# Performance work log

Measured on AMD Instinct MI355X. Metric: run time of the kernel, lower is better.

## Reference

```python
import jax, jax.numpy as jnp
import numpy as np

T, H, I, E, K = 2048, 1024, 768, 16, 4

def setup_inputs() -> dict:
    key = jax.random.key(0)
    k1, k2, k3, k4, k5 = jax.random.split(key, 5)
    hidden_states = jax.random.normal(k1, (T, H), dtype=jnp.float32)
    top_k_index = jax.random.randint(k2, (T, K), 0, E, dtype=jnp.int64)
    top_k_weights = jax.random.uniform(k3, (T, K), dtype=jnp.float32)
    gate_up_proj = jax.random.normal(k4, (E, 2 * I, H), dtype=jnp.float32) * 0.02
    down_proj = jax.random.normal(k5, (E, H, I), dtype=jnp.float32) * 0.02
    return {"hidden_states": hidden_states, "top_k_index": top_k_index,
            "top_k_weights": top_k_weights, "gate_up_proj": gate_up_proj,
            "down_proj": down_proj}

def reference(hidden_states, top_k_index, top_k_weights, gate_up_proj, down_proj):
    # Masked dense MoE: scan over experts, each expert does full-token GEMMs
    # and a per-token combine weight (sum of routing weights where routed to e).
    # index_add over token_idx == sum over k of (mask * weight) * expert_out.
    n_experts = gate_up_proj.shape[0]

    def body(acc, xs):
        w_gu, w_d, e = xs  # [2I,H], [H,I], scalar
        gu = hidden_states @ w_gu.T                 # [T, 2I]
        gate, up = jnp.split(gu, 2, axis=-1)        # [T, I] each
        h = jax.nn.silu(gate) * up                  # [T, I]
        out = h @ w_d.T                             # [T, H]
        w_tok = jnp.sum(jnp.where(top_k_index == e, top_k_weights, 0.0), axis=-1)  # [T]
        return acc + out * w_tok[:, None], None

    acc0 = jnp.zeros_like(hidden_states)
    final, _ = jax.lax.scan(body, acc0, (gate_up_proj, down_proj, jnp.arange(n_experts)))
    return final
```

## Files before the change

kernel.cpp:

```cpp
#include <hip/hip_runtime.h>
#include <hip/hip_bf16.h>
#include <stdint.h>

#define T_TOK 2048
#define H_DIM 1024
#define I_DIM 768
#define E_NUM 16
#define K_TOP 4
#define NSLOT (T_TOK * K_TOP)
#define PSLOT 10240
#define NTILE 80

typedef short  s16x8 __attribute__((ext_vector_type(8)));
typedef float  f32x4 __attribute__((ext_vector_type(4)));
typedef unsigned short u16x8 __attribute__((ext_vector_type(8)));
typedef unsigned int   u32x4 __attribute__((ext_vector_type(4)));

#define MEMFENCE asm volatile("" ::: "memory")

__device__ __forceinline__ void gload16(const void* g, void* l) {
  __builtin_amdgcn_global_load_lds(
      (const __attribute__((address_space(1))) uint32_t*)g,
      (__attribute__((address_space(3))) uint32_t*)l, 16, 0, 0);
}

__device__ __forceinline__ unsigned short f2bf(float f) {
  __hip_bfloat16 h = __float2bfloat16(f);
  return *reinterpret_cast<unsigned short*>(&h);
}

__device__ __forceinline__ unsigned int cvtpk(float lo, float hi) {
  unsigned int r;
  asm("v_cvt_pk_bf16_f32 %0, %1, %2" : "=v"(r) : "v"(lo), "v"(hi));
  return r;
}

__device__ __forceinline__ void write_b_row(char* bregion, int r, int half,
                                            f32x4 f0, f32x4 f1, f32x4 f2, f32x4 f3) {
  union { u32x4 u; u16x8 s; } a_, b_;
  a_.u[0] = cvtpk(f0[0], f0[1]); a_.u[1] = cvtpk(f0[2], f0[3]);
  a_.u[2] = cvtpk(f1[0], f1[1]); a_.u[3] = cvtpk(f1[2], f1[3]);
  b_.u[0] = cvtpk(f2[0], f2[1]); b_.u[1] = cvtpk(f2[2], f2[3]);
  b_.u[2] = cvtpk(f3[0], f3[1]); b_.u[3] = cvtpk(f3[2], f3[3]);
  int xr = (r >> 1) & 3;
  char* wb = bregion + r * 64;
  *(u16x8*)(wb + (((2*half + 0) ^ xr) * 16)) = a_.s;
  *(u16x8*)(wb + (((2*half + 1) ^ xr) * 16)) = b_.s;
}

__global__ __launch_bounds__(256) void cvt_bf16_kernel(
    const float* __restrict__ in, unsigned short* __restrict__ out, int n8) {
  int i = blockIdx.x * 256 + threadIdx.x;
  if (i >= n8) return;
  const float4* p = (const float4*)in;
  float4 a = p[2 * (size_t)i];
  float4 b = p[2 * (size_t)i + 1];
  u16x8 o;
  o[0] = f2bf(a.x); o[1] = f2bf(a.y); o[2] = f2bf(a.z); o[3] = f2bf(a.w);
  o[4] = f2bf(b.x); o[5] = f2bf(b.y); o[6] = f2bf(b.z); o[7] = f2bf(b.w);
  *(u16x8*)(out + (size_t)i * 8) = o;
}

__global__ __launch_bounds__(256) void route_kernel(
    const int* __restrict__ idx, const float* __restrict__ wts,
    int* __restrict__ slot_tok, float* __restrict__ slot_w,
    int* __restrict__ slot_of, int* __restrict__ tile_expert) {
  __shared__ int cnt[256][16];
  __shared__ int tot[16];
  __shared__ int pb[17];
  int tid = threadIdx.x;

  for (int e = 0; e < 16; ++e) cnt[tid][e] = 0;
  const int s0 = tid * 32;
  for (int i = 0; i < 32; ++i) {
    int e = idx[s0 + i] & 15;
    cnt[tid][e]++;
  }
  __syncthreads();
  if (tid < 16) {
    int run = 0;
    for (int c = 0; c < 256; ++c) { int v = cnt[c][tid]; cnt[c][tid] = run; run += v; }
    tot[tid] = run;
  }
  __syncthreads();
  if (tid == 0) {
    int acc = 0;
    for (int e = 0; e < 16; ++e) { pb[e] = acc; acc += (tot[e] + 127) & ~127; }
    pb[16] = acc;
  }
  __syncthreads();
  for (int p = tid; p < PSLOT; p += 256) { slot_tok[p] = 0; slot_w[p] = 0.0f; }
  if (tid < NTILE) {
    int ef = -1;
    for (int e = 0; e < 16; ++e)
      if (tid * 128 >= pb[e] && tid * 128 < pb[e + 1]) ef = e;
    tile_expert[tid] = ef;
  }
  __syncthreads();
  for (int i = 0; i < 32; ++i) {
    int s = s0 + i;
    int e = idx[s] & 15;
    int pos = pb[e] + cnt[tid][e]++;
    slot_tok[pos] = s >> 2;
    slot_w[pos]   = wts[s];
    slot_of[s]    = pos;
  }
}

__global__ __launch_bounds__(512) void gemm1_kernel(
    const unsigned short* __restrict__ Xbf,
    const float* __restrict__ Wgu,
    const int* __restrict__ slot_tok,
    const int* __restrict__ tile_expert,
    unsigned short* __restrict__ hbuf) {
  int bid  = blockIdx.y * 12 + blockIdx.x;
  int sbid = (bid & 7) * 120 + (bid >> 3);
  int by   = sbid / 12;
  int bx   = sbid % 12;
  int e = tile_expert[by];
  if (e < 0) return;
  int m0 = by * 128;
  int t = threadIdx.x;
  int lane = t & 63, w = t >> 6;
  int wr = w >> 2, wc = w & 3;
  int l15 = lane & 15, lhi = lane >> 4;

  __shared__ char lds[2 * 24576];
  char* buf0 = lds;
  char* buf1 = lds + 24576;

  int tokA = slot_tok[m0 + (t >> 2)];
  int aswz = ((t & 3) ^ ((t >> 3) & 3)) * 16;
  const char* gA = (const char*)(Xbf + (size_t)tokA * H_DIM) + aswz;

  int brq = (t & 7) ^ ((t >> 3) & 7);
  int br  = t >> 3;
  const char* gB0 = (const char*)(Wgu + ((size_t)e * 1536 + bx * 64 + br) * H_DIM) + brq * 16;
  const char* gB1 = (const char*)(Wgu + ((size_t)e * 1536 + 768 + bx * 64 + br) * H_DIM) + brq * 16;

  int pswz = (lhi ^ ((l15 >> 1) & 3)) * 8;

  f32x4 accg[4] = {};
  f32x4 accu[4] = {};

#define NT1 32
#define G1_STAGE(bufp, kt) do {                               \
    size_t ao = (size_t)(kt) * 64;                            \
    size_t bo = (size_t)(kt) * 128;                           \
    gload16(gA  + ao, (bufp) + t * 16);                       \
    gload16(gB0 + bo, (bufp) + 8192 + t * 16);                \
    gload16(gB1 + bo, (bufp) + 16384 + t * 16);               \
  } while (0)

#define B_FRAG(dst, cb, rb) do {                                              \
    const char* base_ = (cb) + 8192 + (rb) * 128;                             \
    f32x4 x0_ = *(const f32x4*)(base_ + (((2*lhi    ) ^ ((rb) & 7)) * 16));   \
    f32x4 x1_ = *(const f32x4*)(base_ + (((2*lhi + 1) ^ ((rb) & 7)) * 16));   \
    union { u32x4 u; s16x8 s; } pk_;                                          \
    pk_.u[0] = cvtpk(x0_[0], x0_[1]);                                         \
    pk_.u[1] = cvtpk(x0_[2], x0_[3]);                                         \
    pk_.u[2] = cvtpk(x1_[0], x1_[1]);                                         \
    pk_.u[3] = cvtpk(x1_[2], x1_[3]);                                         \
    dst = pk_.s;                                                              \
  } while (0)

#define G1_COMPUTE(cb) do {                                                            \
    const short* La = (const short*)(cb);                                              \
    s16x8 af[4], bg, bu;                                                               \
    _Pragma("unroll")                                                                  \
    for (int mi = 0; mi < 4; ++mi)                                                     \
      af[mi] = *(const s16x8*)(La + (wr * 64 + mi * 16 + l15) * 32 + pswz);            \
    int rbg = wc * 16 + l15;                                                           \
    B_FRAG(bg, (cb), rbg);                                                             \
    B_FRAG(bu, (cb), rbg + 64);                                                        \
    __builtin_amdgcn_s_setprio(1);                                                     \
    _Pragma("unroll")                                                                  \
    for (int mi = 0; mi < 4; ++mi) {                                                   \
      accg[mi] = __builtin_amdgcn_mfma_f32_16x16x32_bf16(af[mi], bg, accg[mi], 0, 0, 0); \
      accu[mi] = __builtin_amdgcn_mfma_f32_16x16x32_bf16(af[mi], bu, accu[mi], 0, 0, 0); \
    }                                                                                  \
    __builtin_amdgcn_s_setprio(0);                                                     \
  } while (0)

  G1_STAGE(buf0, 0);
  int cur = 0;
  for (int kt = 0; kt < NT1; ++kt) {
    char* cbuf = cur ? buf1 : buf0;
    char* nbuf = cur ? buf0 : buf1;
    if (kt + 1 < NT1) {
      MEMFENCE;
      G1_STAGE(nbuf, kt + 1);
      asm volatile("s_waitcnt vmcnt(3)" ::: "memory");
    } else {
      asm volatile("s_waitcnt vmcnt(0)" ::: "memory");
    }
    __builtin_amdgcn_s_barrier();
    MEMFENCE;
    G1_COMPUTE(cbuf);
    MEMFENCE;
    __builtin_amdgcn_s_barrier();
    cur ^= 1;
  }
#undef G1_STAGE
#undef G1_COMPUTE
#undef B_FRAG

#pragma unroll
  for (int mi = 0; mi < 4; ++mi) {
    int col = bx * 64 + wc * 16 + l15;
#pragma unroll
    for (int q = 0; q < 4; ++q) {
      int m = m0 + wr * 64 + mi * 16 + lhi * 4 + q;
      float g = accg[mi][q];
      float u = accu[mi][q];
      float s = g / (1.0f + __expf(-g));
      hbuf[(size_t)m * I_DIM + col] = f2bf(s * u);
    }
  }
}

__global__ __launch_bounds__(256) void gemm2_kernel(
    const unsigned short* __restrict__ hbuf,
    const float* __restrict__ Wd,
    const int* __restrict__ slot_tok,
    const float* __restrict__ slot_w,
    const int* __restrict__ tile_expert,
    float* __restrict__ y) {
  int bid  = blockIdx.y * 8 + blockIdx.x;
  int sbid = (bid & 7) * 80 + (bid >> 3);
  int by   = sbid >> 3;
  int bx   = sbid & 7;
  int e = tile_expert[by];
  if (e < 0) return;
  int m0 = by * 128;
  int tid = threadIdx.x;
  int lane = tid & 63, w = tid >> 6;
  int wr = w >> 1, wc = w & 1;

  __shared__ short lds[2 * 8192];
  char* buf0 = (char*)lds;
  char* buf1 = buf0 + 16384;

  int srow = tid >> 2;
  int swzc = ((tid & 3) ^ ((tid >> 3) & 3)) * 16;
  const char* gA0 = (const char*)(hbuf + (size_t)(m0 + srow) * I_DIM) + swzc;
  const char* gA1 = (const char*)(hbuf + (size_t)(m0 + 64 + srow) * I_DIM) + swzc;

  int brow = tid >> 1;
  int half = tid & 1;
  const float* gB = Wd + ((size_t)e * 1024 + bx * 128 + brow) * I_DIM + half * 16;

  int pswz = ((lane >> 4) ^ (((lane & 15) >> 1) & 3)) * 8;

  f32x4 acc[4][4] = {};
  f32x4 s0_0, s0_1, s0_2, s0_3, s1_0, s1_1, s1_2, s1_3;
  f32x4 s2_0, s2_1, s2_2, s2_3, s3_0, s3_1, s3_2, s3_3;

#define NT2 24
#define A_GLOAD2(kt, bufp) do {                               \
    int kk_ = (kt) < NT2 ? (kt) : NT2 - 1;                    \
    int ko_ = kk_ * 64;                                       \
    gload16(gA0 + ko_, (bufp) + tid * 16);                    \
    gload16(gA1 + ko_, (bufp) + 4096 + tid * 16);             \
  } while (0)
#define B_LOAD2(v0, v1, v2, v3, kt) do {                      \
    int kk_ = (kt) < NT2 ? (kt) : NT2 - 1;                    \
    const f32x4* p_ = (const f32x4*)(gB + (size_t)kk_ * 32);  \
    v0 = p_[0]; v1 = p_[1]; v2 = p_[2]; v3 = p_[3];           \
  } while (0)

#define G2_COMPUTE(bufp) do {                                                          \
    const short* La = (const short*)(bufp);                                            \
    s16x8 af[4], bf[4];                                                                \
    _Pragma("unroll")                                                                  \
    for (int mi = 0; mi < 4; ++mi)                                                     \
      af[mi] = *(const s16x8*)(La + (wr * 64 + mi * 16 + (lane & 15)) * 32 + pswz);    \
    _Pragma("unroll")                                                                  \
    for (int ni = 0; ni < 4; ++ni)                                                     \
      bf[ni] = *(const s16x8*)(La + 4096 + (wc * 64 + ni * 16 + (lane & 15)) * 32 + pswz); \
    _Pragma("unroll")                                                                  \
    for (int mi = 0; mi < 4; ++mi)                                                     \
      _Pragma("unroll")                                                                \
      for (int ni = 0; ni < 4; ++ni)                                                   \
        acc[mi][ni] = __builtin_amdgcn_mfma_f32_16x16x32_bf16(af[mi], bf[ni], acc[mi][ni], 0, 0, 0); \
  } while (0)

#define ITER2(kt, wv0, wv1, wv2, wv3, lv0, lv1, lv2, lv3) do {  \
    char* cbuf_ = ((kt) & 1) ? buf1 : buf0;                     \
    char* nbuf_ = ((kt) & 1) ? buf0 : buf1;                     \
    MEMFENCE;                                                   \
    A_GLOAD2((kt) + 1, nbuf_);                                  \
    MEMFENCE;                                                   \
    B_LOAD2(lv0, lv1, lv2, lv3, (kt) + 3);                      \
    asm volatile("s_waitcnt vmcnt(10)" ::: "memory");           \
    write_b_row(nbuf_ + 8192, brow, half, wv0, wv1, wv2, wv3);  \
    asm volatile("s_waitcnt lgkmcnt(0)" ::: "memory");          \
    __builtin_amdgcn_s_barrier();                               \
    MEMFENCE;                                                   \
    G2_COMPUTE(cbuf_);                                          \
    MEMFENCE;                                                   \
    __builtin_amdgcn_s_barrier();                               \
  } while (0)

  A_GLOAD2(0, buf0);
  MEMFENCE;
  B_LOAD2(s0_0, s0_1, s0_2, s0_3, 0);
  MEMFENCE;
  B_LOAD2(s1_0, s1_1, s1_2, s1_3, 1);
  MEMFENCE;
  B_LOAD2(s2_0, s2_1, s2_2, s2_3, 2);
  asm volatile("s_waitcnt vmcnt(8)" ::: "memory");
  write_b_row(buf0 + 8192, brow, half, s0_0, s0_1, s0_2, s0_3);

  for (int kt = 0; kt < NT2; kt += 4) {
    ITER2(kt + 0, s1_0, s1_1, s1_2, s1_3, s3_0, s3_1, s3_2, s3_3);
    ITER2(kt + 1, s2_0, s2_1, s2_2, s2_3, s0_0, s0_1, s0_2, s0_3);
    ITER2(kt + 2, s3_0, s3_1, s3_2, s3_3, s1_0, s1_1, s1_2, s1_3);
    ITER2(kt + 3, s0_0, s0_1, s0_2, s0_3, s2_0, s2_1, s2_2, s2_3);
  }
#undef ITER2
#undef G2_COMPUTE
#undef B_LOAD2
#undef A_GLOAD2

#pragma unroll
  for (int mi = 0; mi < 4; ++mi) {
#pragma unroll
    for (int q = 0; q < 4; ++q) {
      int m = m0 + wr * 64 + mi * 16 + (lane >> 4) * 4 + q;
      float wgt = slot_w[m];
      float* orow = y + (size_t)m * H_DIM + bx * 128 + wc * 64 + (lane & 15);
#pragma unroll
      for (int ni = 0; ni < 4; ++ni)
        orow[ni * 16] = acc[mi][ni][q] * wgt;
    }
  }
}

__global__ __launch_bounds__(256) void combine_kernel(
    const float* __restrict__ y, const int* __restrict__ slot_of,
    float* __restrict__ out) {
  int t = blockIdx.x;
  int c = threadIdx.x * 4;
  int s0 = slot_of[t * 4 + 0], s1 = slot_of[t * 4 + 1];
  int s2 = slot_of[t * 4 + 2], s3 = slot_of[t * 4 + 3];
  f32x4 v0 = *(const f32x4*)(y + (size_t)s0 * H_DIM + c);
  f32x4 v1 = *(const f32x4*)(y + (size_t)s1 * H_DIM + c);
  f32x4 v2 = *(const f32x4*)(y + (size_t)s2 * H_DIM + c);
  f32x4 v3 = *(const f32x4*)(y + (size_t)s3 * H_DIM + c);
  f32x4 r = (v0 + v1) + (v2 + v3);
  *(f32x4*)(out + (size_t)t * H_DIM + c) = r;
}

extern "C" void kernel_launch(void* const* d_in, const int* in_sizes, int n_in,
                              void* d_out, int out_size, void* d_ws, size_t ws_size,
                              hipStream_t stream) {
  const float* hs       = (const float*)d_in[0];
  const int*   topk_idx = (const int*)d_in[1];
  const float* topk_w   = (const float*)d_in[2];
  const float* w_gu     = (const float*)d_in[3];
  const float* w_d      = (const float*)d_in[4];
  float* out = (float*)d_out;

  char* ws = (char*)d_ws;
  unsigned short* Xbf  = (unsigned short*)(ws);
  unsigned short* hbuf = (unsigned short*)(ws + 4194304);
  float*          y    = (float*)(ws + 19922944);
  int*   slot_tok    = (int*)(ws + 61865984);
  float* slot_w      = (float*)(ws + 61906944);
  int*   slot_of     = (int*)(ws + 61947904);
  int*   tile_expert = (int*)(ws + 61980672);

  cvt_bf16_kernel<<<1024, 256, 0, stream>>>(hs, Xbf, T_TOK * H_DIM / 8);
  route_kernel<<<1, 256, 0, stream>>>(topk_idx, topk_w, slot_tok, slot_w,
                                      slot_of, tile_expert);

  gemm1_kernel<<<dim3(12, NTILE), 512, 0, stream>>>(Xbf, w_gu, slot_tok, tile_expert, hbuf);
  gemm2_kernel<<<dim3(8, NTILE), 256, 0, stream>>>(hbuf, w_d, slot_tok, slot_w, tile_expert, y);
  combine_kernel<<<T_TOK, 256, 0, stream>>>(y, slot_of, out);
}
```

Baseline: 126.6 us.

## Keep expert gate/up weight slice resident in LDS and loop over token tiles

gemm1 is restructured into one block per (expert, 32-column slice of I). Each block loads its gate and up weight rows once, converts them to bf16 and keeps them in 128KB of swizzled LDS, then loops over all of that expert's 128-row token tiles while streaming only the A operand through a double buffer. This removes the repeated fp32 weight reloads and per-step conversion from every token tile. In exchange the grid shrinks to 384 blocks with uneven work per expert, occupancy is limited by the large LDS footprint, and the per-block weight preload is serial.

```diff
diff --git a/kernel.cpp b/kernel.cpp
--- a/kernel.cpp
+++ b/kernel.cpp
@@ -64,7 +64,8 @@
 __global__ __launch_bounds__(256) void route_kernel(
     const int* __restrict__ idx, const float* __restrict__ wts,
     int* __restrict__ slot_tok, float* __restrict__ slot_w,
-    int* __restrict__ slot_of, int* __restrict__ tile_expert) {
+    int* __restrict__ slot_of, int* __restrict__ tile_expert,
+    int* __restrict__ exp_base) {
   __shared__ int cnt[256][16];
   __shared__ int tot[16];
   __shared__ int pb[17];
@@ -96,6 +97,7 @@
       if (tid * 128 >= pb[e] && tid * 128 < pb[e + 1]) ef = e;
     tile_expert[tid] = ef;
   }
+  if (tid < 17) exp_base[tid] = pb[tid];
   __syncthreads();
   for (int i = 0; i < 32; ++i) {
     int s = s0 + i;
@@ -111,110 +113,110 @@
     const unsigned short* __restrict__ Xbf,
     const float* __restrict__ Wgu,
     const int* __restrict__ slot_tok,
-    const int* __restrict__ tile_expert,
+    const int* __restrict__ exp_base,
     unsigned short* __restrict__ hbuf) {
-  int bid  = blockIdx.y * 12 + blockIdx.x;
-  int sbid = (bid & 7) * 120 + (bid >> 3);
-  int by   = sbid / 12;
-  int bx   = sbid % 12;
-  int e = tile_expert[by];
-  if (e < 0) return;
-  int m0 = by * 128;
+  int p = blockIdx.x;
+  int e = blockIdx.y;
+  int base = exp_base[e], end = exp_base[e + 1];
+  int ntiles = (end - base) >> 7;
+  if (ntiles == 0) return;
   int t = threadIdx.x;
   int lane = t & 63, w = t >> 6;
-  int wr = w >> 2, wc = w & 3;
+  int wr = w >> 1, wc = w & 1;
   int l15 = lane & 15, lhi = lane >> 4;
 
-  __shared__ char lds[2 * 24576];
-  char* buf0 = lds;
-  char* buf1 = lds + 24576;
-
-  int tokA = slot_tok[m0 + (t >> 2)];
+  __shared__ char lds[147456];
+  char* Bl    = lds;
+  char* Abuf0 = lds + 131072;
+  char* Abuf1 = lds + 139264;
+
+  {
+    int r = t >> 3;
+    int grow = e * 1536 + ((r < 32) ? (p * 32 + r) : (768 + p * 32 + (r - 32)));
+    const f32x4* src = (const f32x4*)(Wgu + (size_t)grow * H_DIM + (t & 7) * 128);
+    char* rowb = Bl + r * 2048;
+    int xr = (r & 7) << 4;
+#pragma unroll 4
+    for (int j = 0; j < 16; ++j) {
+      f32x4 a = src[2 * j], b = src[2 * j + 1];
+      union { u32x4 u; u16x8 s; } pk;
+      pk.u[0] = cvtpk(a[0], a[1]); pk.u[1] = cvtpk(a[2], a[3]);
+      pk.u[2] = cvtpk(b[0], b[1]); pk.u[3] = cvtpk(b[2], b[3]);
+      int c16 = (((t & 7) * 16 + j) * 16);
+      *(u16x8*)(rowb + (c16 ^ xr)) = pk.s;
+    }
+  }
+  __syncthreads();
+
+  int arow = t >> 2;
   int aswz = ((t & 3) ^ ((t >> 3) & 3)) * 16;
-  const char* gA = (const char*)(Xbf + (size_t)tokA * H_DIM) + aswz;
-
-  int brq = (t & 7) ^ ((t >> 3) & 7);
-  int br  = t >> 3;
-  const char* gB0 = (const char*)(Wgu + ((size_t)e * 1536 + bx * 64 + br) * H_DIM) + brq * 16;
-  const char* gB1 = (const char*)(Wgu + ((size_t)e * 1536 + 768 + bx * 64 + br) * H_DIM) + brq * 16;
-
   int pswz = (lhi ^ ((l15 >> 1) & 3)) * 8;
 
-  f32x4 accg[4] = {};
-  f32x4 accu[4] = {};
-
-#define NT1 32
-#define G1_STAGE(bufp, kt) do {                               \
-    size_t ao = (size_t)(kt) * 64;                            \
-    size_t bo = (size_t)(kt) * 128;                           \
-    gload16(gA  + ao, (bufp) + t * 16);                       \
-    gload16(gB0 + bo, (bufp) + 8192 + t * 16);                \
-    gload16(gB1 + bo, (bufp) + 16384 + t * 16);               \
-  } while (0)
-
-#define B_FRAG(dst, cb, rb) do {                                              \
-    const char* base_ = (cb) + 8192 + (rb) * 128;                             \
-    f32x4 x0_ = *(const f32x4*)(base_ + (((2*lhi    ) ^ ((rb) & 7)) * 16));   \
-    f32x4 x1_ = *(const f32x4*)(base_ + (((2*lhi + 1) ^ ((rb) & 7)) * 16));   \
-    union { u32x4 u; s16x8 s; } pk_;                                          \
-    pk_.u[0] = cvtpk(x0_[0], x0_[1]);                                         \
-    pk_.u[1] = cvtpk(x0_[2], x0_[3]);                                         \
-    pk_.u[2] = cvtpk(x1_[0], x1_[1]);                                         \
-    pk_.u[3] = cvtpk(x1_[2], x1_[3]);                                         \
-    dst = pk_.s;                                                              \
-  } while (0)
-
-#define G1_COMPUTE(cb) do {                                                            \
-    const short* La = (const short*)(cb);                                              \
-    s16x8 af[4], bg, bu;                                                               \
-    _Pragma("unroll")                                                                  \
-    for (int mi = 0; mi < 4; ++mi)                                                     \
-      af[mi] = *(const s16x8*)(La + (wr * 64 + mi * 16 + l15) * 32 + pswz);            \
-    int rbg = wc * 16 + l15;                                                           \
-    B_FRAG(bg, (cb), rbg);                                                             \
-    B_FRAG(bu, (cb), rbg + 64);                                                        \
-    __builtin_amdgcn_s_setprio(1);                                                     \
-    _Pragma("unroll")                                                                  \
-    for (int mi = 0; mi < 4; ++mi) {                                                   \
-      accg[mi] = __builtin_amdgcn_mfma_f32_16x16x32_bf16(af[mi], bg, accg[mi], 0, 0, 0); \
-      accu[mi] = __builtin_amdgcn_mfma_f32_16x16x32_bf16(af[mi], bu, accu[mi], 0, 0, 0); \
-    }                                                                                  \
-    __builtin_amdgcn_s_setprio(0);                                                     \
-  } while (0)
-
-  G1_STAGE(buf0, 0);
+  const char* gA_cur;
+  const char* gA_next =
+      (const char*)(Xbf + (size_t)slot_tok[base + arow] * H_DIM) + aswz;
+
+  const short* Bs = (const short*)Bl;
+  int rg = wc * 16 + l15;
+  int ru = 32 + wc * 16 + l15;
+  int bswg = (rg & 7) * 8;
+  int bswu = (ru & 7) * 8;
+
+  gA_cur = gA_next;
+  gload16(gA_cur, Abuf0 + t * 16);
+
   int cur = 0;
-  for (int kt = 0; kt < NT1; ++kt) {
-    char* cbuf = cur ? buf1 : buf0;
-    char* nbuf = cur ? buf0 : buf1;
-    if (kt + 1 < NT1) {
+  for (int mt = 0; mt < ntiles; ++mt) {
+    int m0 = base + mt * 128;
+    if (mt + 1 < ntiles)
+      gA_next = (const char*)(Xbf + (size_t)slot_tok[m0 + 128 + arow] * H_DIM) + aswz;
+
+    f32x4 accg0 = {}, accg1 = {}, accu0 = {}, accu1 = {};
+
+    for (int kt = 0; kt < 32; ++kt) {
+      char* cb = cur ? Abuf1 : Abuf0;
+      char* nb = cur ? Abuf0 : Abuf1;
+      if (kt < 31) {
+        MEMFENCE;
+        gload16(gA_cur + (size_t)(kt + 1) * 64, nb + t * 16);
+        asm volatile("s_waitcnt vmcnt(1)" ::: "memory");
+      } else if (mt + 1 < ntiles) {
+        MEMFENCE;
+        gload16(gA_next, nb + t * 16);
+        asm volatile("s_waitcnt vmcnt(1)" ::: "memory");
+      } else {
+        asm volatile("s_waitcnt vmcnt(0)" ::: "memory");
+      }
+      __builtin_amdgcn_s_barrier();
       MEMFENCE;
-      G1_STAGE(nbuf, kt + 1);
-      asm volatile("s_waitcnt vmcnt(3)" ::: "memory");
-    } else {
-      asm volatile("s_waitcnt vmcnt(0)" ::: "memory");
+
+      const short* La = (const short*)cb;
+      s16x8 af0 = *(const s16x8*)(La + (wr * 32 + l15) * 32 + pswz);
+      s16x8 af1 = *(const s16x8*)(La + (wr * 32 + 16 + l15) * 32 + pswz);
+      s16x8 bg = *(const s16x8*)(Bs + rg * 1024 + ((kt * 32 + lhi * 8) ^ bswg));
+      s16x8 bu = *(const s16x8*)(Bs + ru * 1024 + ((kt * 32 + lhi * 8) ^ bswu));
+      __builtin_amdgcn_s_setprio(1);
+      accg0 = __builtin_amdgcn_mfma_f32_16x16x32_bf16(af0, bg, accg0, 0, 0, 0);
+      accg1 = __builtin_amdgcn_mfma_f32_16x16x32_bf16(af1, bg, accg1, 0, 0, 0);
+      accu0 = __builtin_amdgcn_mfma_f32_16x16x32_bf16(af0, bu, accu0, 0, 0, 0);
+      accu1 = __builtin_amdgcn_mfma_f32_16x16x32_bf16(af1, bu, accu1, 0, 0, 0);
+      __builtin_amdgcn_s_setprio(0);
+      MEMFENCE;
+      __builtin_amdgcn_s_barrier();
+      cur ^= 1;
     }
-    __builtin_amdgcn_s_barrier();
-    MEMFENCE;
-    G1_COMPUTE(cbuf);
-    MEMFENCE;
-    __builtin_amdgcn_s_barrier();
-    cur ^= 1;
-  }
-#undef G1_STAGE
-#undef G1_COMPUTE
-#undef B_FRAG
-
-#pragma unroll
-  for (int mi = 0; mi < 4; ++mi) {
-    int col = bx * 64 + wc * 16 + l15;
+    gA_cur = gA_next;
+
+    int col = p * 32 + wc * 16 + l15;
 #pragma unroll
     for (int q = 0; q < 4; ++q) {
-      int m = m0 + wr * 64 + mi * 16 + lhi * 4 + q;
-      float g = accg[mi][q];
-      float u = accu[mi][q];
-      float s = g / (1.0f + __expf(-g));
-      hbuf[(size_t)m * I_DIM + col] = f2bf(s * u);
+      int m0r = m0 + wr * 32 + lhi * 4 + q;
+      float g0 = accg0[q], u0 = accu0[q];
+      float s0v = g0 / (1.0f + __expf(-g0));
+      hbuf[(size_t)m0r * I_DIM + col] = f2bf(s0v * u0);
+      float g1 = accg1[q], u1 = accu1[q];
+      float s1v = g1 / (1.0f + __expf(-g1));
+      hbuf[(size_t)(m0r + 16) * I_DIM + col] = f2bf(s1v * u1);
     }
   }
 }
@@ -370,12 +372,13 @@
   float* slot_w      = (float*)(ws + 61906944);
   int*   slot_of     = (int*)(ws + 61947904);
   int*   tile_expert = (int*)(ws + 61980672);
+  int*   exp_base    = (int*)(ws + 61981056);
 
   cvt_bf16_kernel<<<1024, 256, 0, stream>>>(hs, Xbf, T_TOK * H_DIM / 8);
   route_kernel<<<1, 256, 0, stream>>>(topk_idx, topk_w, slot_tok, slot_w,
-                                      slot_of, tile_expert);
-
-  gemm1_kernel<<<dim3(12, NTILE), 512, 0, stream>>>(Xbf, w_gu, slot_tok, tile_expert, hbuf);
+                                      slot_of, tile_expert, exp_base);
+
+  gemm1_kernel<<<dim3(24, 16), 512, 0, stream>>>(Xbf, w_gu, slot_tok, exp_base, hbuf);
   gemm2_kernel<<<dim3(8, NTILE), 256, 0, stream>>>(hbuf, w_d, slot_tok, slot_w, tile_expert, y);
   combine_kernel<<<T_TOK, 256, 0, stream>>>(y, slot_of, out);
 }
```

Measured after the change: 179.3 us. 1.42x slower.
